# Performance work log

Measured on AMD Instinct MI355X. Metric: run time of the kernel, lower is better.

The kernel has to match this reference:

```python
import jax, jax.numpy as jnp
import numpy as np

N, E, ND, D = 100000, 200000, 128, 32


def linear_bn(x, W, g, b, eps=1e-5):
    # Linear (no bias) followed by BatchNorm1d in training mode (batch stats)
    y = x @ W
    mu = jnp.mean(y, axis=0)
    var = jnp.var(y, axis=0)
    return g * (y - mu) * jax.lax.rsqrt(var + eps) + b


def setup_inputs() -> dict:
    key = jax.random.key(0)
    ks = jax.random.split(key, 16)
    s = 0.05
    return {
        "node": jax.random.normal(ks[0], (N, ND), jnp.float32),
        "edge_index": jax.random.randint(ks[1], (E, 2), 0, N, jnp.int64),
        "edge": jax.random.normal(ks[2], (E, D), jnp.float32),
        "hidden": jax.random.normal(ks[3], (1, E, D), jnp.float32),
        "W1": jax.random.normal(ks[4], (2 * ND, 256), jnp.float32) * s,
        "g1": jnp.ones((256,), jnp.float32), "b1": jnp.zeros((256,), jnp.float32),
        "W2": jax.random.normal(ks[5], (256, 256), jnp.float32) * s,
        "g2": jnp.ones((256,), jnp.float32), "b2": jnp.zeros((256,), jnp.float32),
        "W3": jax.random.normal(ks[6], (256, 128), jnp.float32) * s,
        "g3": jnp.ones((128,), jnp.float32), "b3": jnp.zeros((128,), jnp.float32),
        "W4": jax.random.normal(ks[7], (128, D * D), jnp.float32) * s,
        "g4": jnp.ones((D * D,), jnp.float32), "b4": jnp.zeros((D * D,), jnp.float32),
        "bias": jax.random.uniform(ks[8], (D,), jnp.float32, -1.0 / np.sqrt(D), 1.0 / np.sqrt(D)),
        "W_ih": jax.random.normal(ks[9], (3 * D, D), jnp.float32) * s,
        "W_hh": jax.random.normal(ks[10], (3 * D, D), jnp.float32) * s,
        "b_ih": jnp.zeros((3 * D,), jnp.float32),
        "b_hh": jnp.zeros((3 * D,), jnp.float32),
    }


def reference(node, edge_index, edge, hidden, W1, g1, b1, W2, g2, b2, W3, g3, b3,
              W4, g4, b4, bias, W_ih, W_hh, b_ih, b_hh):
    num_edge, edge_dim = edge.shape
    # gather endpoint node features and concat -> [E, 2*node_dim]
    x_ij = jnp.concatenate([node[edge_index[:, 0]], node[edge_index[:, 1]]], axis=1)
    h = jax.nn.relu(linear_bn(x_ij, W1, g1, b1))
    h = jax.nn.relu(linear_bn(h, W2, g2, b2))
    h = jax.nn.relu(linear_bn(h, W3, g3, b3))
    A = linear_bn(h, W4, g4, b4).reshape(num_edge, edge_dim, edge_dim)
    # per-edge small matmul: [E,1,D] @ [E,D,D] -> [E,D]
    message = jnp.einsum('ed,edf->ef', edge, A)
    message = jax.nn.relu(message + bias)
    # single-step GRU (seq_len=1, edges as batch)
    h0 = hidden[0]
    gi = message @ W_ih.T + b_ih
    gh = h0 @ W_hh.T + b_hh
    i_r, i_z, i_n = jnp.split(gi, 3, axis=1)
    h_r, h_z, h_n = jnp.split(gh, 3, axis=1)
    r = jax.nn.sigmoid(i_r + h_r)
    z = jax.nn.sigmoid(i_z + h_z)
    n = jnp.tanh(i_n + r * h_n)
    h_new = (1.0 - z) * n + z * h0
    return h_new, h_new[None]
```

## Files before the change

kernel.cpp:

```cpp
#include <hip/hip_runtime.h>
#include <hip/hip_fp16.h>

#define NE 200000
#define NT 6250
#define NT64 3125
#define GRAM_BLOCKS 512

__device__ float g_st[21248];
__device__ unsigned short g_c4h[1024];
__device__ int g_flag64;

#define SUM1 (&g_st[0])
#define SQ1  (&g_st[256])
#define SUM2 (&g_st[512])
#define SQ2  (&g_st[768])
#define SUM3 (&g_st[1024])
#define SQ3  (&g_st[1152])
#define GMAT (&g_st[1280])
#define CS3  (&g_st[17664])
#define A1   (&g_st[17792])
#define C1   (&g_st[18048])
#define A2   (&g_st[18304])
#define C2   (&g_st[18560])
#define A3   (&g_st[18816])
#define C3   (&g_st[18944])
#define A4   (&g_st[19072])
#define C4   (&g_st[20096])

typedef unsigned short u16;
typedef _Float16 f16x8 __attribute__((ext_vector_type(8)));
typedef float f32x4 __attribute__((ext_vector_type(4)));

__device__ __forceinline__ f32x4 mfma16(f16x8 a, f16x8 b, f32x4 c) {
  return __builtin_amdgcn_mfma_f32_16x16x32_f16(a, b, c, 0, 0, 0);
}
__device__ __forceinline__ u16 f2h(float x) {
  __half h = __float2half_rn(x);
  return *reinterpret_cast<u16*>(&h);
}
__device__ __forceinline__ float h2f(u16 s) {
  __half h = *reinterpret_cast<__half*>(&s);
  return __half2float(h);
}
__device__ __forceinline__ float relu_np(float t) { return (t < 0.f) ? 0.f : t; }
__device__ __forceinline__ unsigned packh2(float a, float b) {
  return (unsigned)f2h(a) | ((unsigned)f2h(b) << 16);
}

__global__ void GraphConv2_16518444221042_kernel(float* __restrict__ out,
                                                 float v, int n) {
  int i = blockIdx.x * 256 + threadIdx.x;
  if (i < n) out[i] = v;
}

__global__ void k_init(const int* __restrict__ e) {
  int i = blockIdx.x * 256 + threadIdx.x;
  if (i < 17792) g_st[i] = 0.f;
  if (i == 0) {
    int allz = 1;
    for (int k = 1; k < 128; k += 2) allz &= (e[k] == 0);
    g_flag64 = allz;
  }
}

__global__ void k_packA(const float* __restrict__ W1,
                        const float* __restrict__ W2,
                        const float* __restrict__ W3,
                        u16* __restrict__ dst) {
  int i = blockIdx.x * 256 + threadIdx.x;
  if (i >= 163840) return;
  float v;
  if (i < 65536) {
    int n = i >> 8, k = i & 255;
    v = W1[k * 256 + n];
  } else if (i < 131072) {
    int i2 = i - 65536, n = i2 >> 8, k = i2 & 255;
    v = W2[k * 256 + n];
  } else {
    int i2 = i - 131072, n = i2 >> 8, k = i2 & 255;
    v = W3[k * 128 + n];
  }
  dst[i] = f2h(v);
}

__global__ void k_packB(const float* __restrict__ W4,
                        const float* __restrict__ Wih,
                        const float* __restrict__ Whh,
                        u16* __restrict__ dst) {
  int i = blockIdx.x * 256 + threadIdx.x;
  if (i >= 137216) return;
  float v;
  if (i < 131072) {
    int n = i >> 7, k = i & 127;
    v = W4[(size_t)k * 1024 + n];
  } else if (i < 134144) {
    v = Wih[i - 131072];
  } else {
    v = Whh[i - 134144];
  }
  dst[i] = f2h(v);
}

__global__ void k_finalize(const float* __restrict__ g,
                           const float* __restrict__ b, int which, int C) {
  int j = threadIdx.x;
  if (j < C) {
    const float* sum = (which == 1) ? SUM1 : (which == 2) ? SUM2 : SUM3;
    const float* sq  = (which == 1) ? SQ1 : (which == 2) ? SQ2 : SQ3;
    float* aa = (which == 1) ? A1 : (which == 2) ? A2 : A3;
    float* cc = (which == 1) ? C1 : (which == 2) ? C2 : C3;
    const float invE = 1.f / (float)NE;
    float mu = sum[j] * invE;
    float var = fmaf(-mu, mu, sq[j] * invE);
    float s = rsqrtf(var + 1e-5f);
    float av = g[j] * s;
    aa[j] = av;
    cc[j] = fmaf(-av, mu, b[j]);
  }
}

__global__ __launch_bounds__(64) void k_finalize4(
    const float* __restrict__ W4, const float* __restrict__ g4,
    const float* __restrict__ b4) {
  __shared__ float wsh[128];
  const int lane = threadIdx.x;
  const float invE = 1.f / (float)NE;
  for (int j = blockIdx.x; j < 1024; j += gridDim.x) {
    float w0 = W4[lane * 1024 + j];
    float w1 = W4[(lane + 64) * 1024 + j];
    wsh[lane] = w0;
    wsh[lane + 64] = w1;
    __syncthreads();
    float s0 = 0.f, s1 = 0.f;
#pragma unroll 8
    for (int k = 0; k < 128; ++k) {
      float wk = wsh[k];
      s0 = fmaf(GMAT[lane * 128 + k], wk, s0);
      s1 = fmaf(GMAT[(lane + 64) * 128 + k], wk, s1);
    }
    float acc = w0 * s0 + w1 * s1;
    float mac = CS3[lane] * w0 + CS3[lane + 64] * w1;
#pragma unroll
    for (int off = 32; off > 0; off >>= 1) {
      acc += __shfl_down(acc, off);
      mac += __shfl_down(mac, off);
    }
    if (lane == 0) {
      float mu = mac * invE;
      float var = fmaf(-mu, mu, acc * invE);
      float s = rsqrtf(var + 1e-5f);
      float av = g4[j] * s;
      A4[j] = av;
      float cv = fmaf(-av, mu, b4[j]);
      C4[j] = cv;
      g_c4h[(j & 31) * 32 + (j >> 5)] = f2h(cv);
    }
    __syncthreads();
  }
}

template <int L>
__global__ __launch_bounds__(512) void k_gemmP(
    const float* __restrict__ node, const int* __restrict__ eidx,
    const u16* __restrict__ Yin, const u16* __restrict__ Wt,
    u16* __restrict__ Yout) {
  constexpr int CN = (L == 3) ? 128 : 256;
  constexpr int CTW = CN / 128;
  constexpr int LDH = 264;
  __shared__ __align__(16) u16 H[2][64 * LDH];
  __shared__ float csum_s[CN], csq_s[CN];
  const int tid = threadIdx.x;
  float* SUMo = (L == 1) ? SUM1 : (L == 2) ? SUM2 : SUM3;
  float* SQo  = (L == 1) ? SQ1 : (L == 2) ? SQ2 : SQ3;
  const float* Ain = (L == 2) ? A1 : A2;
  const float* Cin = (L == 2) ? C1 : C2;

  const int l = tid & 63, w = tid >> 6;
  const int lr = l & 15, lg = l >> 4;
  const int is64 = g_flag64;

  f16x8 bfr[CTW][8];
#pragma unroll
  for (int c = 0; c < CTW; ++c)
#pragma unroll
    for (int kb = 0; kb < 8; ++kb)
      bfr[c][kb] = *(const f16x8*)&Wt[(size_t)((w * CTW + c) * 16 + lr) * 256 +
                                      kb * 32 + lg * 8];

  if (tid < CN) { csum_s[tid] = 0.f; csq_s[tid] = 0.f; }
  float sreg[CTW] = {}, qreg[CTW] = {};

  float4 ldf[8];
  uint4 ldi[4];

  {
    const int r0 = blockIdx.x * 64;
    if constexpr (L == 1) {
#pragma unroll
      for (int i = 0; i < 8; ++i) {
        int idx = tid + i * 512;
        int row = idx >> 6, col = (idx & 63) * 4;
        int sel = col >> 7, kc = col & 127;
        int j = (r0 + row) * 2 + sel;
        int v = is64 ? eidx[j * 2] : eidx[j];
        v = v < 0 ? 0 : (v > 99999 ? 99999 : v);
        ldf[i] = *(const float4*)&node[(size_t)v * 128 + kc];
      }
    } else {
#pragma unroll
      for (int i = 0; i < 4; ++i) {
        int idx = tid + i * 512;
        int row = idx >> 5, col = (idx & 31) * 8;
        ldi[i] = *(const uint4*)&Yin[(size_t)(r0 + row) * 256 + col];
      }
    }
  }

  int cur = 0;
  for (int t = blockIdx.x; t < NT64; t += gridDim.x) {
    const int r0 = t * 64;
    const int tn = t + gridDim.x;
    if constexpr (L == 1) {
#pragma unroll
      for (int i = 0; i < 8; ++i) {
        int idx = tid + i * 512;
        int row = idx >> 6, col = (idx & 63) * 4;
        uint2 pk;
        pk.x = packh2(ldf[i].x, ldf[i].y);
        pk.y = packh2(ldf[i].z, ldf[i].w);
        *(uint2*)&H[cur][row * LDH + col] = pk;
      }
    } else {
#pragma unroll
      for (int i = 0; i < 4; ++i) {
        int idx = tid + i * 512;
        int row = idx >> 5, col = (idx & 31) * 8;
        const u16* sp = (const u16*)&ldi[i];
        uint4 o;
        unsigned po[4];
#pragma unroll
        for (int p = 0; p < 4; ++p) {
          float v0 = relu_np(fmaf(Ain[col + 2 * p], h2f(sp[2 * p]),
                                  Cin[col + 2 * p]));
          float v1 = relu_np(fmaf(Ain[col + 2 * p + 1], h2f(sp[2 * p + 1]),
                                  Cin[col + 2 * p + 1]));
          po[p] = packh2(v0, v1);
        }
        o.x = po[0]; o.y = po[1]; o.z = po[2]; o.w = po[3];
        *(uint4*)&H[cur][row * LDH + col] = o;
      }
    }
    if (tn < NT64) {
      const int rn = tn * 64;
      if constexpr (L == 1) {
#pragma unroll
        for (int i = 0; i < 8; ++i) {
          int idx = tid + i * 512;
          int row = idx >> 6, col = (idx & 63) * 4;
          int sel = col >> 7, kc = col & 127;
          int j = (rn + row) * 2 + sel;
          int v = is64 ? eidx[j * 2] : eidx[j];
          v = v < 0 ? 0 : (v > 99999 ? 99999 : v);
          ldf[i] = *(const float4*)&node[(size_t)v * 128 + kc];
        }
      } else {
#pragma unroll
        for (int i = 0; i < 4; ++i) {
          int idx = tid + i * 512;
          int row = idx >> 5, col = (idx & 31) * 8;
          ldi[i] = *(const uint4*)&Yin[(size_t)(rn + row) * 256 + col];
        }
      }
    }
    __syncthreads();

    f32x4 acc[4][CTW] = {};
#pragma unroll
    for (int kb = 0; kb < 8; ++kb) {
      f16x8 a[4];
#pragma unroll
      for (int rt = 0; rt < 4; ++rt)
        a[rt] = *(const f16x8*)&H[cur][(rt * 16 + lr) * LDH + kb * 32 + lg * 8];
#pragma unroll
      for (int c = 0; c < CTW; ++c)
#pragma unroll
        for (int rt = 0; rt < 4; ++rt)
          acc[rt][c] = mfma16(a[rt], bfr[c][kb], acc[rt][c]);
    }

#pragma unroll
    for (int c = 0; c < CTW; ++c) {
      const int col = (w * CTW + c) * 16 + lr;
#pragma unroll
      for (int rt = 0; rt < 4; ++rt)
#pragma unroll
        for (int r = 0; r < 4; ++r) {
          float v = acc[rt][c][r];
          sreg[c] += v;
          qreg[c] = fmaf(v, v, qreg[c]);
          int row = rt * 16 + lg * 4 + r;
          Yout[(size_t)(r0 + row) * CN + col] = f2h(v);
        }
    }
    cur ^= 1;
  }

  __syncthreads();
#pragma unroll
  for (int c = 0; c < CTW; ++c) {
    const int col = (w * CTW + c) * 16 + lr;
    atomicAdd(&csum_s[col], sreg[c]);
    atomicAdd(&csq_s[col], qreg[c]);
  }
  __syncthreads();
  if (tid < CN) {
    atomicAdd(&SUMo[tid], csum_s[tid]);
    atomicAdd(&SQo[tid], csq_s[tid]);
  }
}

__global__ __launch_bounds__(256, 2) void k_gram_m(const u16* __restrict__ y3g,
                                                   float* __restrict__ pg) {
  __shared__ u16 h3T[128 * 40];
  __shared__ float cred[128];
  const int tid = threadIdx.x;
  const int l = tid & 63, w = tid >> 6;
  const int lr = l & 15, lg = l >> 4;
  const int c4 = (tid & 31) * 4;
  const int rb = tid >> 5;
  f32x4 acc[2][8] = {};
  float csc[4] = {0.f, 0.f, 0.f, 0.f};

  for (int t = blockIdx.x; t < NT; t += gridDim.x) {
    const size_t r0 = (size_t)t * 32;
    __syncthreads();
#pragma unroll
    for (int i = 0; i < 4; ++i) {
      int row = rb + i * 8;
      ushort4 v = *(const ushort4*)&y3g[(r0 + row) * 128 + c4];
      float h[4];
      h[0] = relu_np(fmaf(A3[c4 + 0], h2f(v.x), C3[c4 + 0]));
      h[1] = relu_np(fmaf(A3[c4 + 1], h2f(v.y), C3[c4 + 1]));
      h[2] = relu_np(fmaf(A3[c4 + 2], h2f(v.z), C3[c4 + 2]));
      h[3] = relu_np(fmaf(A3[c4 + 3], h2f(v.w), C3[c4 + 3]));
#pragma unroll
      for (int j = 0; j < 4; ++j) {
        csc[j] += h[j];
        int col = c4 + j;
        int swz = ((col >> 2) & 3) << 3;
        h3T[col * 40 + (row ^ swz)] = f2h(h[j]);
      }
    }
    __syncthreads();
    f16x8 bfr[8];
#pragma unroll
    for (int tj = 0; tj < 8; ++tj) {
      int col = tj * 16 + lr;
      int swz = ((col >> 2) & 3) << 3;
      bfr[tj] = *(const f16x8*)&h3T[col * 40 + ((lg * 8) ^ swz)];
    }
#pragma unroll
    for (int ri = 0; ri < 2; ++ri) {
      f16x8 a = bfr[w * 2 + ri];
#pragma unroll
      for (int tj = 0; tj < 8; ++tj)
        acc[ri][tj] = mfma16(a, bfr[tj], acc[ri][tj]);
    }
  }
  float* my = pg + (size_t)blockIdx.x * 16384;
#pragma unroll
  for (int ri = 0; ri < 2; ++ri)
#pragma unroll
    for (int tj = 0; tj < 8; ++tj)
#pragma unroll
      for (int r = 0; r < 4; ++r) {
        int row = (w * 2 + ri) * 16 + lg * 4 + r, col = tj * 16 + lr;
        my[row * 128 + col] = acc[ri][tj][r];
      }
  if (tid < 128) cred[tid] = 0.f;
  __syncthreads();
#pragma unroll
  for (int j = 0; j < 4; ++j) atomicAdd(&cred[c4 + j], csc[j]);
  __syncthreads();
  if (tid < 128) atomicAdd(&CS3[tid], cred[tid]);
}

__global__ void k_gramred(const float* __restrict__ pg) {
  int g = blockIdx.x * 256 + threadIdx.x;
  float s = 0.f;
  for (int p = 0; p < GRAM_BLOCKS; ++p) s += pg[(size_t)p * 16384 + g];
  GMAT[g] = s;
}

__global__ __launch_bounds__(256, 4) void k_final64(
    const u16* __restrict__ y3g, const u16* __restrict__ w4t,
    const u16* __restrict__ wihh, const u16* __restrict__ whhh,
    const float* __restrict__ edge, const float* __restrict__ hidden,
    const float* __restrict__ bias, const float* __restrict__ bih,
    const float* __restrict__ bhh, float* __restrict__ out) {
  __shared__ __align__(16) u16 H3[64 * 136];
  __shared__ __align__(16) u16 SLAB[32 * 136];
  __shared__ __align__(16) u16 EDS[64 * 40];
  float* OUTBUF = (float*)H3;
  u16* MSGu = H3 + 4096;
  const int tid = threadIdx.x;
  const size_t r0 = (size_t)blockIdx.x * 64;

#pragma unroll
  for (int i = 0; i < 8; ++i) {
    int idx = tid + i * 256;
    int row = idx >> 5, col = (idx & 31) * 4;
    ushort4 v = *(const ushort4*)&y3g[(r0 + row) * 128 + col];
    float h0 = relu_np(fmaf(A3[col + 0], h2f(v.x), C3[col + 0]));
    float h1 = relu_np(fmaf(A3[col + 1], h2f(v.y), C3[col + 1]));
    float h2v = relu_np(fmaf(A3[col + 2], h2f(v.z), C3[col + 2]));
    float h3v = relu_np(fmaf(A3[col + 3], h2f(v.w), C3[col + 3]));
    uint2 pk;
    pk.x = packh2(h0, h1);
    pk.y = packh2(h2v, h3v);
    *(uint2*)&H3[row * 136 + col] = pk;
  }
#pragma unroll
  for (int i = 0; i < 2; ++i) {
    int idx = tid + i * 256;
    int row = idx >> 3, col = (idx & 7) * 4;
    float4 ev = *(const float4*)&edge[(r0 + row) * 32 + col];
    uint2 pe;
    pe.x = packh2(ev.x, ev.y);
    pe.y = packh2(ev.z, ev.w);
    *(uint2*)&EDS[row * 40 + col] = pe;
  }
  __syncthreads();

  const int l = tid & 63, w = tid >> 6;
  const int lr = l & 15, lg = l >> 4;
  f16x8 af[4];
#pragma unroll
  for (int kb = 0; kb < 4; ++kb)
    af[kb] = *(const f16x8*)&H3[(w * 16 + lr) * 136 + kb * 32 + lg * 8];

  float mp[4][2] = {};
  for (int cg = 0; cg < 32; ++cg) {
    __syncthreads();
    {
      int c = tid >> 3, ch = tid & 7;
#pragma unroll
      for (int q = 0; q < 2; ++q) {
        int kk = (ch + q * 8) * 8;
        *(uint4*)&SLAB[c * 136 + kk] =
            *(const uint4*)&w4t[(size_t)(cg * 32 + c) * 128 + kk];
      }
    }
    __syncthreads();
#pragma unroll
    for (int ci = 0; ci < 2; ++ci) {
      f16x8 b[4];
#pragma unroll
      for (int kb = 0; kb < 4; ++kb)
        b[kb] = *(const f16x8*)&SLAB[(ci * 16 + lr) * 136 + kb * 32 + lg * 8];
      const float a4v = A4[cg * 32 + ci * 16 + lr];
      f32x4 acc = {0.f, 0.f, 0.f, 0.f};
#pragma unroll
      for (int kb = 0; kb < 4; ++kb) acc = mfma16(af[kb], b[kb], acc);
#pragma unroll
      for (int r = 0; r < 4; ++r) {
        int e = w * 16 + lg * 4 + r;
        float ed = h2f(EDS[e * 40 + cg]);
        mp[r][ci] = fmaf(ed * a4v, acc[r], mp[r][ci]);
      }
    }
  }

  f32x4 m0[2];
  {
    f16x8 ae = *(const f16x8*)&EDS[(w * 16 + lr) * 40 + lg * 8];
#pragma unroll
    for (int ci = 0; ci < 2; ++ci) {
      f16x8 bc = *(const f16x8*)&g_c4h[(ci * 16 + lr) * 32 + lg * 8];
      f32x4 z = {0.f, 0.f, 0.f, 0.f};
      m0[ci] = mfma16(ae, bc, z);
    }
  }
#pragma unroll
  for (int ci = 0; ci < 2; ++ci)
#pragma unroll
    for (int r = 0; r < 4; ++r) {
      int e = w * 16 + lg * 4 + r;
      int f = ci * 16 + lr;
      float v = relu_np(mp[r][ci] + m0[ci][r] + bias[f]);
      MSGu[e * 40 + f] = f2h(v);
    }
  __syncthreads();

  f16x8 am = *(const f16x8*)&MSGu[(w * 16 + lr) * 40 + lg * 8];
  f16x8 ah;
  {
    int e = w * 16 + lr;
    float4 h0a = *(const float4*)&hidden[(r0 + e) * 32 + lg * 8];
    float4 h0b = *(const float4*)&hidden[(r0 + e) * 32 + lg * 8 + 4];
    union { unsigned u[4]; f16x8 h; } uu;
    uu.u[0] = packh2(h0a.x, h0a.y);
    uu.u[1] = packh2(h0a.z, h0a.w);
    uu.u[2] = packh2(h0b.x, h0b.y);
    uu.u[3] = packh2(h0b.z, h0b.w);
    ah = uu.h;
  }
  f32x4 gi[6], gh[6];
#pragma unroll
  for (int ct = 0; ct < 6; ++ct) {
    f16x8 bi = *(const f16x8*)&wihh[(ct * 16 + lr) * 32 + lg * 8];
    f16x8 bh = *(const f16x8*)&whhh[(ct * 16 + lr) * 32 + lg * 8];
    f32x4 z = {0.f, 0.f, 0.f, 0.f};
    gi[ct] = mfma16(am, bi, z);
    gh[ct] = mfma16(ah, bh, z);
  }
#pragma unroll
  for (int r = 0; r < 4; ++r) {
    int e = w * 16 + lg * 4 + r;
#pragma unroll
    for (int hf = 0; hf < 2; ++hf) {
      int f = hf * 16 + lr;
      float xr = gi[hf][r] + bih[f];
      float xz = gi[2 + hf][r] + bih[32 + f];
      float xn = gi[4 + hf][r] + bih[64 + f];
      float hr = gh[hf][r] + bhh[f];
      float hz = gh[2 + hf][r] + bhh[32 + f];
      float hn = gh[4 + hf][r] + bhh[64 + f];
      float rg = 1.f / (1.f + __expf(-(xr + hr)));
      float zg = 1.f / (1.f + __expf(-(xz + hz)));
      float ng = tanhf(fmaf(rg, hn, xn));
      float h0v = hidden[(r0 + e) * 32 + f];
      OUTBUF[e * 32 + f] = fmaf(zg, h0v - ng, ng);
    }
  }
  __syncthreads();
#pragma unroll
  for (int i = 0; i < 2; ++i) {
    int off = tid * 4 + i * 1024;
    size_t g = r0 * 32 + off;
    float4 v = *(const float4*)&OUTBUF[off];
    *(float4*)&out[g] = v;
    *(float4*)&out[(size_t)NE * 32 + g] = v;
  }
}

extern "C" void kernel_launch(void* const* d_in, const int* in_sizes, int n_in,
                              void* d_out, int out_size, void* d_ws,
                              size_t ws_size, hipStream_t stream) {
  float* out = (float*)d_out;

  static const int EXP[21] = {
      12800000, 400000, 6400000, 6400000,
      65536, 256, 256, 65536, 256, 256, 32768, 128, 128,
      131072, 1024, 1024, 32, 3072, 3072, 96, 96};
  int bad = -1;
  if (n_in != 21) bad = 25;
  else
    for (int i = 0; i < 21; ++i)
      if (in_sizes[i] != EXP[i]) { bad = i; break; }
  if (bad < 0 && out_size != 12800000) bad = 22;
  const size_t Y1B = (size_t)NE * 256 * 2;
  if (bad < 0 && (!d_ws || ws_size < 2 * Y1B)) bad = 24;
  if (bad >= 0) {
    float code = 3.0e7f + (float)bad * 1.0e6f;
    GraphConv2_16518444221042_kernel<<<(out_size + 255) / 256, 256, 0, stream>>>(
        out, code, out_size);
    return;
  }

  const float* node   = (const float*)d_in[0];
  const int*   eidx   = (const int*)d_in[1];
  const float* edge   = (const float*)d_in[2];
  const float* hidden = (const float*)d_in[3];
  const float* W1 = (const float*)d_in[4];
  const float* g1 = (const float*)d_in[5];
  const float* b1 = (const float*)d_in[6];
  const float* W2 = (const float*)d_in[7];
  const float* g2 = (const float*)d_in[8];
  const float* b2 = (const float*)d_in[9];
  const float* W3 = (const float*)d_in[10];
  const float* g3 = (const float*)d_in[11];
  const float* b3 = (const float*)d_in[12];
  const float* W4 = (const float*)d_in[13];
  const float* g4 = (const float*)d_in[14];
  const float* b4 = (const float*)d_in[15];
  const float* bias = (const float*)d_in[16];
  const float* Wih = (const float*)d_in[17];
  const float* Whh = (const float*)d_in[18];
  const float* bih = (const float*)d_in[19];
  const float* bhh = (const float*)d_in[20];

  u16* y1 = (u16*)d_ws;
  u16* y2 = (u16*)d_ws + (size_t)NE * 256;
  u16* y3 = (u16*)d_ws;

  u16* pkA = (u16*)d_out;
  u16* w1t = pkA;
  u16* w2t = pkA + 65536;
  u16* w3t = pkA + 131072;
  u16* w4t  = y2;
  u16* wihh = y2 + 131072;
  u16* whhh = y2 + 134144;
  float* pgram = (float*)(y2 + 2097152);

  k_init<<<70, 256, 0, stream>>>(eidx);
  k_packA<<<640, 256, 0, stream>>>(W1, W2, W3, pkA);

  k_gemmP<1><<<512, 512, 0, stream>>>(node, eidx, nullptr, w1t, y1);
  k_finalize<<<1, 256, 0, stream>>>(g1, b1, 1, 256);
  k_gemmP<2><<<512, 512, 0, stream>>>(nullptr, nullptr, y1, w2t, y2);
  k_finalize<<<1, 256, 0, stream>>>(g2, b2, 2, 256);
  k_gemmP<3><<<512, 512, 0, stream>>>(nullptr, nullptr, y2, w3t, y3);
  k_finalize<<<1, 256, 0, stream>>>(g3, b3, 3, 128);
  k_packB<<<537, 256, 0, stream>>>(W4, Wih, Whh, y2);
  k_gram_m<<<GRAM_BLOCKS, 256, 0, stream>>>(y3, pgram);
  k_gramred<<<64, 256, 0, stream>>>(pgram);
  k_finalize4<<<128, 64, 0, stream>>>(W4, g4, b4);
  k_final64<<<NT64, 256, 0, stream>>>(y3, w4t, wihh, whhh, edge, hidden,
                                      bias, bih, bhh, out);
}
```

Before: 424.1 us.

## Double-buffer W4 slabs with register prefetch and fold BN scale into packed W4

The final kernel now keeps two shared-memory slabs for W4 columns. It prefetches the next slab's global loads into registers while computing on the current one, which removes one barrier per iteration. The per-column BN scale A4 is folded into the fp16 packed W4 weights, so k_packB is moved after k_finalize4 to make A4 available. The edge values are also hoisted out of the inner ci loop. This costs extra shared memory and registers, which may lower occupancy, and applies the scale before fp16 rounding.

```diff
diff --git a/kernel.cpp b/kernel.cpp
--- a/kernel.cpp
+++ b/kernel.cpp
@@ -92,7 +92,7 @@
   float v;
   if (i < 131072) {
     int n = i >> 7, k = i & 127;
-    v = W4[(size_t)k * 1024 + n];
+    v = W4[(size_t)k * 1024 + n] * A4[n];
   } else if (i < 134144) {
     v = Wih[i - 131072];
   } else {
@@ -399,7 +399,7 @@
     const float* __restrict__ bias, const float* __restrict__ bih,
     const float* __restrict__ bhh, float* __restrict__ out) {
   __shared__ __align__(16) u16 H3[64 * 136];
-  __shared__ __align__(16) u16 SLAB[32 * 136];
+  __shared__ __align__(16) u16 SLAB[2][32 * 136];
   __shared__ __align__(16) u16 EDS[64 * 40];
   float* OUTBUF = (float*)H3;
   u16* MSGu = H3 + 4096;
@@ -439,36 +439,40 @@
   for (int kb = 0; kb < 4; ++kb)
     af[kb] = *(const f16x8*)&H3[(w * 16 + lr) * 136 + kb * 32 + lg * 8];
 
+  const int sc = tid >> 3, sch = tid & 7;
+  uint4 pre0 = *(const uint4*)&w4t[(size_t)sc * 128 + sch * 8];
+  uint4 pre1 = *(const uint4*)&w4t[(size_t)sc * 128 + (sch + 8) * 8];
+
   float mp[4][2] = {};
+  int cur = 0;
   for (int cg = 0; cg < 32; ++cg) {
+    *(uint4*)&SLAB[cur][sc * 136 + sch * 8] = pre0;
+    *(uint4*)&SLAB[cur][sc * 136 + (sch + 8) * 8] = pre1;
+    if (cg + 1 < 32) {
+      pre0 = *(const uint4*)&w4t[(size_t)((cg + 1) * 32 + sc) * 128 + sch * 8];
+      pre1 =
+          *(const uint4*)&w4t[(size_t)((cg + 1) * 32 + sc) * 128 + (sch + 8) * 8];
+    }
     __syncthreads();
-    {
-      int c = tid >> 3, ch = tid & 7;
-#pragma unroll
-      for (int q = 0; q < 2; ++q) {
-        int kk = (ch + q * 8) * 8;
-        *(uint4*)&SLAB[c * 136 + kk] =
-            *(const uint4*)&w4t[(size_t)(cg * 32 + c) * 128 + kk];
-      }
-    }
-    __syncthreads();
+    float edv[4];
+#pragma unroll
+    for (int r = 0; r < 4; ++r)
+      edv[r] = h2f(EDS[(w * 16 + lg * 4 + r) * 40 + cg]);
 #pragma unroll
     for (int ci = 0; ci < 2; ++ci) {
       f16x8 b[4];
 #pragma unroll
       for (int kb = 0; kb < 4; ++kb)
-        b[kb] = *(const f16x8*)&SLAB[(ci * 16 + lr) * 136 + kb * 32 + lg * 8];
-      const float a4v = A4[cg * 32 + ci * 16 + lr];
+        b[kb] =
+            *(const f16x8*)&SLAB[cur][(ci * 16 + lr) * 136 + kb * 32 + lg * 8];
       f32x4 acc = {0.f, 0.f, 0.f, 0.f};
 #pragma unroll
       for (int kb = 0; kb < 4; ++kb) acc = mfma16(af[kb], b[kb], acc);
 #pragma unroll
-      for (int r = 0; r < 4; ++r) {
-        int e = w * 16 + lg * 4 + r;
-        float ed = h2f(EDS[e * 40 + cg]);
-        mp[r][ci] = fmaf(ed * a4v, acc[r], mp[r][ci]);
-      }
-    }
+      for (int r = 0; r < 4; ++r)
+        mp[r][ci] = fmaf(edv[r], acc[r], mp[r][ci]);
+    }
+    cur ^= 1;
   }
 
   f32x4 m0[2];
@@ -612,10 +616,10 @@
   k_finalize<<<1, 256, 0, stream>>>(g2, b2, 2, 256);
   k_gemmP<3><<<512, 512, 0, stream>>>(nullptr, nullptr, y2, w3t, y3);
   k_finalize<<<1, 256, 0, stream>>>(g3, b3, 3, 128);
-  k_packB<<<537, 256, 0, stream>>>(W4, Wih, Whh, y2);
   k_gram_m<<<GRAM_BLOCKS, 256, 0, stream>>>(y3, pgram);
   k_gramred<<<64, 256, 0, stream>>>(pgram);
   k_finalize4<<<128, 64, 0, stream>>>(W4, g4, b4);
+  k_packB<<<537, 256, 0, stream>>>(W4, Wih, Whh, y2);
   k_final64<<<NT64, 256, 0, stream>>>(y3, w4t, wihh, whhh, edge, hidden,
                                       bias, bih, bhh, out);
 }
```

After: 417.9 us. No clear change (-1.5%).
